# Kernel optimization log

Measured on AMD Instinct MI355X. Metric: run time of the kernel, lower is better.

## Reference

```python
import jax, jax.numpy as jnp
import numpy as np


def setup_inputs() -> dict:
    key = jax.random.key(0)
    kq, kk, kv = jax.random.split(key, 3)
    shape = (4, 16, 2048, 128)  # [B, H, S, D]
    return {
        "query": jax.random.normal(kq, shape, dtype=jnp.float32),
        "key": jax.random.normal(kk, shape, dtype=jnp.float32),
        "value": jax.random.normal(kv, shape, dtype=jnp.float32),
    }


def reference(query, key, value):
    # NOTE: the original torch code computes math.sqrt(d) but immediately
    # overwrites it with d itself, so the scale is 1/D (not 1/sqrt(D)).
    d = query.shape[-1]
    score = jnp.einsum("bhqd,bhkd->bhqk", query, key) / d  # [B,H,S,S]
    attn = jax.nn.softmax(score, axis=-1)
    return jnp.einsum("bhqk,bhkd->bhqd", attn, value)
```

## Files before the change

kernel.cpp:

```cpp
#include <hip/hip_runtime.h>
#include <stdint.h>

typedef __bf16 bf16x8 __attribute__((ext_vector_type(8)));
typedef float  f32x4  __attribute__((ext_vector_type(4)));

#define DEVI __device__ __forceinline__

constexpr int Bc = 4, Hc = 16, Ss = 2048, Dd = 128;
constexpr int BH = Bc * Hc;
constexpr int BM = 128;
constexpr int BN = 64;
constexpr int NTIL = Ss / BN;
constexpr int LDP = 72;
constexpr float SCALE = 1.0f / 128.0f;

constexpr int SK_OFF = 0;
constexpr int SV_OFF = 16 * 1024;
constexpr int SP_OFF = 32 * 1024;
constexpr int LDS_BYTES = SP_OFF + BM * LDP * 2;
static_assert(LDS_BYTES <= 53 * 1024, "need 3 blocks/CU");

DEVI unsigned short f2bf_bits(float x) {
  unsigned u = __builtin_bit_cast(unsigned, x);
  u += 0x7fffu + ((u >> 16) & 1u);
  return (unsigned short)(u >> 16);
}
DEVI __bf16 f2bf(float x) {
  unsigned short b = f2bf_bits(x);
  return __builtin_bit_cast(__bf16, b);
}
DEVI unsigned pk_bf16(float a, float b) {
  return (unsigned)f2bf_bits(a) | ((unsigned)f2bf_bits(b) << 16);
}

DEVI void gload_lds16(const void* g, void* l) {
  __builtin_amdgcn_global_load_lds(
      (const __attribute__((address_space(1))) unsigned*)(uintptr_t)g,
      (__attribute__((address_space(3))) unsigned*)(unsigned)(uintptr_t)l,
      16, 0, 0);
}

__global__ void k_conv_bf16(const float* __restrict__ in, __bf16* __restrict__ out,
                            int n4) {
  int i = blockIdx.x * blockDim.x + threadIdx.x;
  const int stride = gridDim.x * blockDim.x;
  for (; i < n4; i += stride) {
    float4 v = ((const float4*)in)[i];
    ushort4 o;
    o.x = f2bf_bits(v.x); o.y = f2bf_bits(v.y);
    o.z = f2bf_bits(v.z); o.w = f2bf_bits(v.w);
    ((ushort4*)out)[i] = o;
  }
}

__global__ void k_vtrans(const float* __restrict__ v, __bf16* __restrict__ vt) {
  constexpr int LDT = 130;
  __shared__ __bf16 tile[64 * LDT];
  const int bh = blockIdx.y;
  const int s0 = blockIdx.x * 64;
  const int u = threadIdx.x;
  const float4* src = (const float4*)(v + ((size_t)bh * Ss + s0) * Dd);
  #pragma unroll
  for (int i = 0; i < 8; i++) {
    int f = i * 256 + u;
    int row = f >> 5;
    int c4 = (f & 31) << 2;
    float4 x = src[f];
    tile[row * LDT + c4 + 0] = f2bf(x.x);
    tile[row * LDT + c4 + 1] = f2bf(x.y);
    tile[row * LDT + c4 + 2] = f2bf(x.z);
    tile[row * LDT + c4 + 3] = f2bf(x.w);
  }
  __syncthreads();
  const int c = u & 7;
  const int dl = u >> 3;
  #pragma unroll
  for (int it = 0; it < 4; it++) {
    const int d = it * 32 + dl;
    bf16x8 o;
    #pragma unroll
    for (int e = 0; e < 8; e++) o[e] = tile[(c * 8 + e) * LDT + d];
    *(bf16x8*)(vt + ((size_t)bh * Dd + d) * Ss + s0 + c * 8) = o;
  }
}

__launch_bounds__(256, 3)
__global__ void k_flash(const float* __restrict__ Q, const __bf16* __restrict__ Kb,
                        const __bf16* __restrict__ Vt, float* __restrict__ O) {
  __shared__ __align__(16) char lds[LDS_BYTES];
  char* sK = lds + SK_OFF;
  char* sV = lds + SV_OFF;
  unsigned short* sP = (unsigned short*)(lds + SP_OFF);

  const int tid = threadIdx.x;
  const int w = tid >> 6;
  const int lane = tid & 63;
  const int quad = lane >> 4;
  const int l16 = lane & 15;

  const int bx = blockIdx.x;
  const int bh = bx & (BH - 1);
  const int q0 = (bx >> 6) * BM;

  bf16x8 qa[2][4];
  {
    const float* qb = Q + ((size_t)bh * Ss + q0 + w * 32) * Dd;
    #pragma unroll
    for (int mt = 0; mt < 2; mt++)
      #pragma unroll
      for (int kk = 0; kk < 4; kk++) {
        const float* p = qb + (mt * 16 + l16) * Dd + kk * 32 + quad * 8;
        float4 a = ((const float4*)p)[0];
        float4 b = ((const float4*)p)[1];
        bf16x8 f;
        f[0] = f2bf(a.x * SCALE); f[1] = f2bf(a.y * SCALE);
        f[2] = f2bf(a.z * SCALE); f[3] = f2bf(a.w * SCALE);
        f[4] = f2bf(b.x * SCALE); f[5] = f2bf(b.y * SCALE);
        f[6] = f2bf(b.z * SCALE); f[7] = f2bf(b.w * SCALE);
        qa[mt][kk] = f;
      }
  }

  f32x4 acc[2][8];
  #pragma unroll
  for (int mt = 0; mt < 2; mt++)
    #pragma unroll
    for (int dt = 0; dt < 8; dt++)
      acc[mt][dt] = (f32x4){0.f, 0.f, 0.f, 0.f};

  float lacc[2] = {0.f, 0.f};

  const __bf16* kbh = Kb + (size_t)bh * Ss * Dd;
  const __bf16* vbh = Vt + (size_t)bh * Ss * Dd;

  for (int t = 0; t < NTIL; t++) {
    const int n0 = t * BN;
    #pragma unroll
    for (int f = 0; f < 4; f++) {
      const int fk = w * 4 + f;
      const __bf16* g = kbh + (size_t)(n0 + (fk & 3) * 16 + l16) * Dd
                        + (fk >> 2) * 32 + quad * 8;
      gload_lds16(g, sK + fk * 1024 + lane * 16);
    }
    #pragma unroll
    for (int f = 0; f < 4; f++) {
      const int fv = w * 4 + f;
      const __bf16* g = vbh + (size_t)((fv & 7) * 16 + l16) * Ss
                        + n0 + (fv >> 3) * 32 + quad * 8;
      gload_lds16(g, sV + fv * 1024 + lane * 16);
    }
    __syncthreads();

    f32x4 sc[2][4];
    #pragma unroll
    for (int mt = 0; mt < 2; mt++)
      #pragma unroll
      for (int nt = 0; nt < 4; nt++)
        sc[mt][nt] = (f32x4){0.f, 0.f, 0.f, 0.f};
    #pragma unroll
    for (int kk = 0; kk < 4; kk++)
      #pragma unroll
      for (int nt = 0; nt < 4; nt++) {
        bf16x8 bk = *(const bf16x8*)(sK + (kk * 4 + nt) * 1024 + lane * 16);
        sc[0][nt] = __builtin_amdgcn_mfma_f32_16x16x32_bf16(bk, qa[0][kk], sc[0][nt], 0, 0, 0);
        sc[1][nt] = __builtin_amdgcn_mfma_f32_16x16x32_bf16(bk, qa[1][kk], sc[1][nt], 0, 0, 0);
      }

    #pragma unroll
    for (int mt = 0; mt < 2; mt++)
      #pragma unroll
      for (int nt = 0; nt < 4; nt++) {
        float p0 = __expf(sc[mt][nt][0]);
        float p1 = __expf(sc[mt][nt][1]);
        float p2 = __expf(sc[mt][nt][2]);
        float p3 = __expf(sc[mt][nt][3]);
        lacc[mt] += (p0 + p1) + (p2 + p3);
        uint2 pw;
        pw.x = pk_bf16(p0, p1);
        pw.y = pk_bf16(p2, p3);
        *(uint2*)(sP + (w * 32 + mt * 16 + l16) * LDP + nt * 16 + quad * 4) = pw;
      }

    #pragma unroll
    for (int kk2 = 0; kk2 < 2; kk2++) {
      bf16x8 pa[2];
      #pragma unroll
      for (int mt = 0; mt < 2; mt++)
        pa[mt] = *(const bf16x8*)((const char*)sP +
                 ((size_t)((w * 32 + mt * 16 + l16) * LDP + kk2 * 32 + quad * 8) * 2));
      #pragma unroll
      for (int dt = 0; dt < 8; dt++) {
        bf16x8 bv = *(const bf16x8*)(sV + (kk2 * 8 + dt) * 1024 + lane * 16);
        acc[0][dt] = __builtin_amdgcn_mfma_f32_16x16x32_bf16(pa[0], bv, acc[0][dt], 0, 0, 0);
        acc[1][dt] = __builtin_amdgcn_mfma_f32_16x16x32_bf16(pa[1], bv, acc[1][dt], 0, 0, 0);
      }
    }
    __syncthreads();
  }

  float inv_l[2][4];
  #pragma unroll
  for (int mt = 0; mt < 2; mt++) {
    float l = lacc[mt];
    l += __shfl_xor(l, 16);
    l += __shfl_xor(l, 32);
    #pragma unroll
    for (int r = 0; r < 4; r++) {
      float lr = __shfl(l, (lane & 48) | (quad * 4 + r));
      inv_l[mt][r] = 1.0f / lr;
    }
  }

  float* ob = O + ((size_t)bh * Ss + q0 + w * 32) * Dd;
  #pragma unroll
  for (int mt = 0; mt < 2; mt++)
    #pragma unroll
    for (int r = 0; r < 4; r++) {
      const float inv = inv_l[mt][r];
      const int row = mt * 16 + quad * 4 + r;
      #pragma unroll
      for (int dt = 0; dt < 8; dt++)
        ob[row * Dd + dt * 16 + l16] = acc[mt][dt][r] * inv;
    }
}

extern "C" void kernel_launch(void* const* d_in, const int* in_sizes, int n_in,
                              void* d_out, int out_size, void* d_ws, size_t ws_size,
                              hipStream_t stream) {
  const float* Q = (const float*)d_in[0];
  const float* K = (const float*)d_in[1];
  const float* V = (const float*)d_in[2];
  float* O = (float*)d_out;
  const size_t elems = (size_t)BH * Ss * Dd;
  __bf16* Kb = (__bf16*)d_ws;
  __bf16* Vt = Kb + elems;

  k_conv_bf16<<<4096, 256, 0, stream>>>(K, Kb, (int)(elems / 4));
  k_vtrans<<<dim3(Ss / 64, BH), 256, 0, stream>>>(V, Vt);
  k_flash<<<dim3((Ss / BM) * BH), 256, 0, stream>>>(Q, Kb, Vt, O);
}
```

Baseline: 399.4 us.

## Double query tile to 256 rows with 512 threads, exp2 softmax, swizzled P

```diff
diff --git a/kernel.cpp b/kernel.cpp
--- a/kernel.cpp
+++ b/kernel.cpp
@@ -8,17 +8,16 @@
 
 constexpr int Bc = 4, Hc = 16, Ss = 2048, Dd = 128;
 constexpr int BH = Bc * Hc;
-constexpr int BM = 128;
+constexpr int BM = 256;
 constexpr int BN = 64;
 constexpr int NTIL = Ss / BN;
-constexpr int LDP = 72;
-constexpr float SCALE = 1.0f / 128.0f;
+constexpr float QSCALE = (1.0f / 128.0f) * 1.4426950408889634f;
 
 constexpr int SK_OFF = 0;
 constexpr int SV_OFF = 16 * 1024;
 constexpr int SP_OFF = 32 * 1024;
-constexpr int LDS_BYTES = SP_OFF + BM * LDP * 2;
-static_assert(LDS_BYTES <= 53 * 1024, "need 3 blocks/CU");
+constexpr int LDS_BYTES = SP_OFF + BM * 128;
+static_assert(LDS_BYTES == 65536, "layout");
 
 DEVI unsigned short f2bf_bits(float x) {
   unsigned u = __builtin_bit_cast(unsigned, x);
@@ -29,8 +28,17 @@
   unsigned short b = f2bf_bits(x);
   return __builtin_bit_cast(__bf16, b);
 }
-DEVI unsigned pk_bf16(float a, float b) {
-  return (unsigned)f2bf_bits(a) | ((unsigned)f2bf_bits(b) << 16);
+DEVI unsigned pk_bf16_rhu(float a, float b) {
+  unsigned ua = __builtin_bit_cast(unsigned, a) + 0x8000u;
+  unsigned ub = __builtin_bit_cast(unsigned, b) + 0x8000u;
+  return __builtin_amdgcn_perm(ub, ua, 0x07060302u);
+}
+DEVI float fast_exp2(float x) {
+#if __has_builtin(__builtin_amdgcn_exp2f)
+  return __builtin_amdgcn_exp2f(x);
+#else
+  return __expf(x * 0.6931471805599453f);
+#endif
 }
 
 DEVI void gload_lds16(const void* g, void* l) {
@@ -41,15 +49,19 @@
 }
 
 __global__ void k_conv_bf16(const float* __restrict__ in, __bf16* __restrict__ out,
-                            int n4) {
+                            int n8) {
   int i = blockIdx.x * blockDim.x + threadIdx.x;
   const int stride = gridDim.x * blockDim.x;
-  for (; i < n4; i += stride) {
-    float4 v = ((const float4*)in)[i];
-    ushort4 o;
-    o.x = f2bf_bits(v.x); o.y = f2bf_bits(v.y);
-    o.z = f2bf_bits(v.z); o.w = f2bf_bits(v.w);
-    ((ushort4*)out)[i] = o;
+  for (; i < n8; i += stride) {
+    float4 a = ((const float4*)in)[2 * i];
+    float4 b = ((const float4*)in)[2 * i + 1];
+    ushort4 o0, o1;
+    o0.x = f2bf_bits(a.x); o0.y = f2bf_bits(a.y);
+    o0.z = f2bf_bits(a.z); o0.w = f2bf_bits(a.w);
+    o1.x = f2bf_bits(b.x); o1.y = f2bf_bits(b.y);
+    o1.z = f2bf_bits(b.z); o1.w = f2bf_bits(b.w);
+    ((ushort4*)out)[2 * i] = o0;
+    ((ushort4*)out)[2 * i + 1] = o1;
   }
 }
 
@@ -84,19 +96,20 @@
   }
 }
 
-__launch_bounds__(256, 3)
+__launch_bounds__(512, 4)
 __global__ void k_flash(const float* __restrict__ Q, const __bf16* __restrict__ Kb,
                         const __bf16* __restrict__ Vt, float* __restrict__ O) {
   __shared__ __align__(16) char lds[LDS_BYTES];
   char* sK = lds + SK_OFF;
   char* sV = lds + SV_OFF;
-  unsigned short* sP = (unsigned short*)(lds + SP_OFF);
+  char* sP = lds + SP_OFF;
 
   const int tid = threadIdx.x;
   const int w = tid >> 6;
   const int lane = tid & 63;
   const int quad = lane >> 4;
   const int l16 = lane & 15;
+  const int sw = l16 & 7;
 
   const int bx = blockIdx.x;
   const int bh = bx & (BH - 1);
@@ -113,10 +126,10 @@
         float4 a = ((const float4*)p)[0];
         float4 b = ((const float4*)p)[1];
         bf16x8 f;
-        f[0] = f2bf(a.x * SCALE); f[1] = f2bf(a.y * SCALE);
-        f[2] = f2bf(a.z * SCALE); f[3] = f2bf(a.w * SCALE);
-        f[4] = f2bf(b.x * SCALE); f[5] = f2bf(b.y * SCALE);
-        f[6] = f2bf(b.z * SCALE); f[7] = f2bf(b.w * SCALE);
+        f[0] = f2bf(a.x * QSCALE); f[1] = f2bf(a.y * QSCALE);
+        f[2] = f2bf(a.z * QSCALE); f[3] = f2bf(a.w * QSCALE);
+        f[4] = f2bf(b.x * QSCALE); f[5] = f2bf(b.y * QSCALE);
+        f[6] = f2bf(b.z * QSCALE); f[7] = f2bf(b.w * QSCALE);
         qa[mt][kk] = f;
       }
   }
@@ -136,15 +149,15 @@
   for (int t = 0; t < NTIL; t++) {
     const int n0 = t * BN;
     #pragma unroll
-    for (int f = 0; f < 4; f++) {
-      const int fk = w * 4 + f;
+    for (int f = 0; f < 2; f++) {
+      const int fk = w * 2 + f;
       const __bf16* g = kbh + (size_t)(n0 + (fk & 3) * 16 + l16) * Dd
                         + (fk >> 2) * 32 + quad * 8;
       gload_lds16(g, sK + fk * 1024 + lane * 16);
     }
     #pragma unroll
-    for (int f = 0; f < 4; f++) {
-      const int fv = w * 4 + f;
+    for (int f = 0; f < 2; f++) {
+      const int fv = w * 2 + f;
       const __bf16* g = vbh + (size_t)((fv & 7) * 16 + l16) * Ss
                         + n0 + (fv >> 3) * 32 + quad * 8;
       gload_lds16(g, sV + fv * 1024 + lane * 16);
@@ -170,24 +183,29 @@
     for (int mt = 0; mt < 2; mt++)
       #pragma unroll
       for (int nt = 0; nt < 4; nt++) {
-        float p0 = __expf(sc[mt][nt][0]);
-        float p1 = __expf(sc[mt][nt][1]);
-        float p2 = __expf(sc[mt][nt][2]);
-        float p3 = __expf(sc[mt][nt][3]);
+        float p0 = fast_exp2(sc[mt][nt][0]);
+        float p1 = fast_exp2(sc[mt][nt][1]);
+        float p2 = fast_exp2(sc[mt][nt][2]);
+        float p3 = fast_exp2(sc[mt][nt][3]);
         lacc[mt] += (p0 + p1) + (p2 + p3);
         uint2 pw;
-        pw.x = pk_bf16(p0, p1);
-        pw.y = pk_bf16(p2, p3);
-        *(uint2*)(sP + (w * 32 + mt * 16 + l16) * LDP + nt * 16 + quad * 4) = pw;
+        pw.x = pk_bf16_rhu(p0, p1);
+        pw.y = pk_bf16_rhu(p2, p3);
+        const int row = w * 32 + mt * 16 + l16;
+        const int g = 2 * nt + (quad >> 1);
+        const int sub = (quad & 1) * 8;
+        *(uint2*)(sP + row * 128 + ((g ^ sw) * 16) + sub) = pw;
       }
 
     #pragma unroll
     for (int kk2 = 0; kk2 < 2; kk2++) {
       bf16x8 pa[2];
       #pragma unroll
-      for (int mt = 0; mt < 2; mt++)
-        pa[mt] = *(const bf16x8*)((const char*)sP +
-                 ((size_t)((w * 32 + mt * 16 + l16) * LDP + kk2 * 32 + quad * 8) * 2));
+      for (int mt = 0; mt < 2; mt++) {
+        const int row = w * 32 + mt * 16 + l16;
+        const int g = kk2 * 4 + quad;
+        pa[mt] = *(const bf16x8*)(sP + row * 128 + ((g ^ sw) * 16));
+      }
       #pragma unroll
       for (int dt = 0; dt < 8; dt++) {
         bf16x8 bv = *(const bf16x8*)(sV + (kk2 * 8 + dt) * 1024 + lane * 16);
@@ -235,7 +253,7 @@
   __bf16* Kb = (__bf16*)d_ws;
   __bf16* Vt = Kb + elems;
 
-  k_conv_bf16<<<4096, 256, 0, stream>>>(K, Kb, (int)(elems / 4));
+  k_conv_bf16<<<4096, 256, 0, stream>>>(K, Kb, (int)(elems / 8));
   k_vtrans<<<dim3(Ss / 64, BH), 256, 0, stream>>>(V, Vt);
-  k_flash<<<dim3((Ss / BM) * BH), 256, 0, stream>>>(Q, Kb, Vt, O);
-}
+  k_flash<<<dim3((Ss / BM) * BH), 512, 0, stream>>>(Q, Kb, Vt, O);
+}
```

Measured after the change: 673.9 us. 68.7% more time.
